# Kernel tuning notes

Hardware: AMD Instinct MI355X
Metric: run time of the kernel (lower is better)

Reference implementation:

```python
import jax, jax.numpy as jnp
import numpy as np

N = 100000      # nodes
E = 1600000     # edges
F_IN = 512      # num_feat
HID = 128       # hidden dim (hardcoded in GNN)
ENC = 64        # encoder_dim
NCLS = 10       # num_classes
DOM = 40        # domain head hidden (hardcoded)


def setup_inputs() -> dict:
    key = jax.random.key(0)
    ks = jax.random.split(key, 16)
    def lin(k, fi, fo):
        kw, kb = jax.random.split(k)
        s = 1.0 / np.sqrt(fi)
        return (jax.random.uniform(kw, (fi, fo), jnp.float32, -s, s),
                jax.random.uniform(kb, (fo,), jnp.float32, -s, s))
    W1, b1 = lin(ks[0], F_IN, HID)
    W2, b2 = lin(ks[1], HID, ENC)
    att_w, att_b = lin(ks[2], ENC, 1)
    cls_w, cls_b = lin(ks[3], ENC, NCLS)
    dw1, db1 = lin(ks[4], ENC, DOM)
    dw2, db2 = lin(ks[5], DOM, 2)
    return {
        "x": jax.random.normal(ks[6], (N, F_IN), jnp.float32),
        "edge_index": jax.random.randint(ks[7], (2, E), 0, N, jnp.int64),
        "ppmi_edge_weight": jax.random.uniform(ks[8], (E,), jnp.float32, 0.01, 1.0),
        "rate": 1,
        "W1": W1, "b1": b1, "W2": W2, "b2": b2,
        "att_w": att_w, "att_b": att_b,
        "cls_w": cls_w, "cls_b": cls_b,
        "dw1": dw1, "db1": db1, "dw2": dw2, "db2": db2,
    }


def _edge_norm(src, dst, w):
    # symmetric normalization d^-1/2 * w * d^-1/2 (self-loops already included)
    deg = jax.ops.segment_sum(w, dst, num_segments=N)
    dinv = jnp.where(deg > 0, jax.lax.rsqrt(deg), 0.0)
    return dinv[src] * w * dinv[dst]


def _conv(h, W, b, src, dst, enorm):
    h = h @ W                                   # [N, out]
    msg = h[src] * enorm[:, None]               # [E+N, out] gather
    return jax.ops.segment_sum(msg, dst, num_segments=N) + b


def _encode(x, src, dst, enorm, W1, b1, W2, b2):
    h = jax.nn.relu(_conv(x, W1, b1, src, dst, enorm))  # dropout = identity (eval)
    return _conv(h, W2, b2, src, dst, enorm)


def reference(x, edge_index, ppmi_edge_weight, rate,
              W1, b1, W2, b2, att_w, att_b,
              cls_w, cls_b, dw1, db1, dw2, db2):
    loop = jnp.arange(N, dtype=edge_index.dtype)
    src = jnp.concatenate([edge_index[0], loop])
    dst = jnp.concatenate([edge_index[1], loop])
    ones_w = jnp.ones(src.shape[0], jnp.float32)
    ppmi_w = jnp.concatenate([ppmi_edge_weight, jnp.ones(N, jnp.float32)])

    gcn_norm = _edge_norm(src, dst, ones_w)
    ppmi_norm = _edge_norm(src, dst, ppmi_w)

    # both encoders share weights (base_model=self.encoder)
    g = _encode(x, src, dst, gcn_norm, W1, b1, W2, b2)    # [N, ENC]
    p = _encode(x, src, dst, ppmi_norm, W1, b1, W2, b2)   # [N, ENC]

    stacked = jnp.stack([g, p], axis=1)                   # [N, 2, ENC]
    logits = stacked @ att_w + att_b                      # [N, 2, 1]
    wts = jax.nn.softmax(logits, axis=1)
    emb = jnp.sum(stacked * wts, axis=1)                  # [N, ENC]

    class_predict = emb @ cls_w + cls_b
    r = jnp.float32(rate)
    # gradient reversal: identity fwd, -rate * grad bwd
    rev = jax.lax.stop_gradient((1.0 + r) * emb) - r * emb
    h = jax.nn.relu(rev @ dw1 + db1)                      # dropout = identity (eval)
    domain_predict = h @ dw2 + db2
    return emb, class_predict, domain_predict
```

## Files before the change

### kernel.cpp

```cpp
#include <hip/hip_runtime.h>
#include <math.h>
#include <stdint.h>

#define NND  100000
#define NED  1600000
#define FIN  512
#define HID  128
#define ENC  64
#define NCLS 10
#define DOM  40

#define SCAN_BS 256
#define NBS ((NND + SCAN_BS - 1) / SCAN_BS)

#define NGEMM 1563
#define NDEG  521
#define NPH1  (NGEMM + NDEG)

typedef __attribute__((ext_vector_type(8))) short short8v;
typedef __attribute__((ext_vector_type(8))) unsigned short ushort8v;
typedef __attribute__((ext_vector_type(4))) float f32x4;
typedef __attribute__((ext_vector_type(4))) unsigned int uint4v;


__device__ inline void split8(const float4 a, const float4 b,
                              short8v& hi, short8v& lo) {
  float f[8] = {a.x, a.y, a.z, a.w, b.x, b.y, b.z, b.w};
  uint4v H, L;
#pragma unroll
  for (int i = 0; i < 4; ++i) {
    unsigned int u0 = __float_as_uint(f[2 * i]);
    unsigned int u1 = __float_as_uint(f[2 * i + 1]);
    H[i] = (u0 >> 16) | (u1 & 0xffff0000u);
    float l0 = f[2 * i]     - __uint_as_float(u0 & 0xffff0000u);
    float l1 = f[2 * i + 1] - __uint_as_float(u1 & 0xffff0000u);
    L[i] = (__float_as_uint(l0) >> 16) | (__float_as_uint(l1) & 0xffff0000u);
  }
  hi = __builtin_bit_cast(short8v, H);
  lo = __builtin_bit_cast(short8v, L);
}

__device__ inline ushort f2bf_rne(float x) {
  unsigned int u = __float_as_uint(x);
  unsigned int r = u + 0x7fffu + ((u >> 16) & 1u);
  return (ushort)(r >> 16);
}

__device__ inline float bf2f(unsigned short v) {
  return __uint_as_float((unsigned int)v << 16);
}

__device__ inline void gload_lds16(const float* gp, float* lp) {
  __builtin_amdgcn_global_load_lds(
      (const __attribute__((address_space(1))) void*)gp,
      (__attribute__((address_space(3))) void*)lp, 16, 0, 0);
}


__global__ void k_prep(const float* __restrict__ W1, ushort* __restrict__ b1hi,
                       const float* __restrict__ W2,
                       ushort* __restrict__ b2hi, ushort* __restrict__ b2lo,
                       unsigned int* __restrict__ packed, int* __restrict__ cursor) {
  int id = blockIdx.x * 256 + threadIdx.x;
  if (id == 0) *cursor = 0;
  if (id < NND) packed[id] = 0u;
  if (id < FIN * HID) {
    int k = id / HID, c = id % HID;
    size_t o = ((size_t)(k >> 3) * HID + c) * 8 + (k & 7);
    b1hi[o] = f2bf_rne(W1[id]);
  } else {
    int id2 = id - FIN * HID;
    if (id2 >= HID * ENC) return;
    int k = id2 / ENC, c = id2 % ENC;
    float x = W2[id2];
    unsigned int u = __float_as_uint(x);
    ushort h = (ushort)(u >> 16);
    float lo = x - __uint_as_float(u & 0xffff0000u);
    ushort l = (ushort)(__float_as_uint(lo) >> 16);
    size_t o = ((size_t)(k >> 3) * ENC + c) * 8 + (k & 7);
    b2hi[o] = h;
    b2lo[o] = l;
  }
}


__global__ __launch_bounds__(256, 4) void k_phase1(
    const float* __restrict__ A, const ushort* __restrict__ Bhi,
    ushort* __restrict__ C,
    const int* __restrict__ dst, const float* __restrict__ ppmi,
    unsigned int* __restrict__ packed, ushort* __restrict__ rank) {
  __shared__ float At[2][64 * 32];
  const int bi = blockIdx.x;
  const int tid = threadIdx.x;

  if ((bi & 3) == 0) {
    for (int e = (bi >> 2) * 256 + tid; e < NED; e += NDEG * 256) {
      int d = dst[e];
      unsigned int fx = (unsigned int)(ppmi[e] * 262144.0f + 0.5f);
      unsigned int v = (1u << 25) | fx;
      unsigned int old = atomicAdd(&packed[d], v);
      rank[e] = (ushort)(old >> 25);
    }
    return;
  }

  const int gb = bi - (bi >> 2) - 1;
  const int lane = tid & 63;
  const int w = tid >> 6;
  const int wr = w >> 1, wc = w & 1;
  const int g = lane >> 4;
  const int l16 = lane & 15;
  const int row_base = gb * 64;

  size_t srow[2]; int scol[2];
#pragma unroll
  for (int i = 0; i < 2; ++i) {
    int ee = i * 1024 + tid * 4;
    int r = ee >> 5;
    int chunk_lds = (ee >> 2) & 7;
    int chunk_g = chunk_lds ^ (r & 7);
    int rr = row_base + r; if (rr >= NND) rr = NND - 1;
    srow[i] = (size_t)rr * FIN;
    scol[i] = chunk_g * 4;
  }

  int coln[4];
#pragma unroll
  for (int n = 0; n < 4; ++n) coln[n] = wc * 64 + n * 16 + l16;
  int arow_l[2];
#pragma unroll
  for (int m = 0; m < 2; ++m) arow_l[m] = wr * 32 + m * 16 + l16;

  f32x4 acc[2][4] = {};

#pragma unroll
  for (int i = 0; i < 2; ++i)
    gload_lds16(A + srow[i] + 0 + scol[i], &At[0][i * 1024 + tid * 4]);
  __syncthreads();

  for (int t = 0; t < FIN / 32; ++t) {
    const int cur = t & 1;
    if (t + 1 < FIN / 32) {
      const int k0n = (t + 1) * 32;
#pragma unroll
      for (int i = 0; i < 2; ++i)
        gload_lds16(A + srow[i] + k0n + scol[i], &At[cur ^ 1][i * 1024 + tid * 4]);
    }

    short8v ah[2], al[2];
#pragma unroll
    for (int m = 0; m < 2; ++m) {
      int r = arow_l[m];
      int c0 = (((g * 2)     ^ (r & 7)) << 2);
      int c1 = (((g * 2 + 1) ^ (r & 7)) << 2);
      float4 a0 = *(const float4*)&At[cur][r * 32 + c0];
      float4 a1 = *(const float4*)&At[cur][r * 32 + c1];
      split8(a0, a1, ah[m], al[m]);
    }

    short8v bh[4];
    const int kc = t * 4 + g;
#pragma unroll
    for (int n = 0; n < 4; ++n)
      bh[n] = *(const short8v*)(Bhi + ((size_t)kc * HID + coln[n]) * 8);

#pragma unroll
    for (int m = 0; m < 2; ++m)
#pragma unroll
      for (int n = 0; n < 4; ++n) {
        acc[m][n] = __builtin_amdgcn_mfma_f32_16x16x32_bf16(ah[m], bh[n], acc[m][n], 0, 0, 0);
        acc[m][n] = __builtin_amdgcn_mfma_f32_16x16x32_bf16(al[m], bh[n], acc[m][n], 0, 0, 0);
      }

    __syncthreads();
  }

#pragma unroll
  for (int m = 0; m < 2; ++m)
#pragma unroll
    for (int i = 0; i < 4; ++i) {
      int r = row_base + wr * 32 + m * 16 + g * 4 + i;
      if (r < NND) {
#pragma unroll
        for (int n = 0; n < 4; ++n)
          C[(size_t)r * HID + coln[n]] = f2bf_rne(acc[m][n][i]);
      }
    }
}


__global__ void k_dinv_alloc(const unsigned int* __restrict__ packed,
                             float* __restrict__ dinv_g, float* __restrict__ dinv_p,
                             int* __restrict__ row_ptr, int* __restrict__ cursor) {
  __shared__ int s[SCAN_BS];
  __shared__ int base;
  int t = threadIdx.x, i = blockIdx.x * SCAN_BS + t;
  int cnt = 0;
  if (i < NND) {
    unsigned int pk = packed[i];
    cnt = (int)(pk >> 25);
    float dp = (float)(pk & 0x1FFFFFFu) * (1.0f / 262144.0f);
    dinv_g[i] = 1.0f / sqrtf((float)cnt + 1.0f);
    dinv_p[i] = 1.0f / sqrtf(dp + 1.0f);
  }
  s[t] = cnt;
  __syncthreads();
  for (int o = 1; o < SCAN_BS; o <<= 1) {
    int add = (t >= o) ? s[t - o] : 0;
    __syncthreads();
    s[t] += add;
    __syncthreads();
  }
  if (t == SCAN_BS - 1) base = atomicAdd(cursor, s[t]);
  __syncthreads();
  if (i < NND) row_ptr[i] = base + s[t] - cnt;
}


__global__ void k_scatter(const int* __restrict__ src, const int* __restrict__ dst,
                          const float* __restrict__ ppmi,
                          const int* __restrict__ row_ptr, const ushort* __restrict__ rank,
                          const float* __restrict__ dinv_g, const float* __restrict__ dinv_p,
                          int2* __restrict__ csr) {
  int e = blockIdx.x * blockDim.x + threadIdx.x;
  if (e >= NED) return;
  int s = src[e], d = dst[e];
  int pos = row_ptr[d] + (int)rank[e];
  ushort gn = f2bf_rne(dinv_g[s] * dinv_g[d]);
  ushort pn = f2bf_rne(dinv_p[s] * ppmi[e] * dinv_p[d]);
  int2 rec;
  rec.x = s;
  rec.y = (int)gn | ((int)pn << 16);
  csr[pos] = rec;
}


__global__ __launch_bounds__(256, 4) void gemm2_split(
    const ushort* __restrict__ As, const ushort* __restrict__ Bhi,
    const ushort* __restrict__ Blo, ushort* __restrict__ C,
    int M, int K, int Nc) {
  const int lane = threadIdx.x & 63;
  const int w = threadIdx.x >> 6;
  const int g = lane >> 4;
  const int l16 = lane & 15;
  const int row_base = blockIdx.x * 128 + w * 32;

  size_t arow[2];
#pragma unroll
  for (int m = 0; m < 2; ++m) {
    int r = row_base + m * 16 + l16;
    if (r >= M) r = M - 1;
    arow[m] = (size_t)r * K;
  }
  int coln[4];
#pragma unroll
  for (int n = 0; n < 4; ++n) coln[n] = n * 16 + l16;

  f32x4 acc[2][4] = {};

  for (int k0 = 0; k0 < K; k0 += 32) {
    short8v ah[2];
#pragma unroll
    for (int m = 0; m < 2; ++m)
      ah[m] = *(const short8v*)(As + arow[m] + k0 + g * 8);
    short8v bh[4], bl[4];
    const int kc = (k0 >> 3) + g;
#pragma unroll
    for (int n = 0; n < 4; ++n) {
      size_t off = ((size_t)kc * Nc + coln[n]) * 8;
      bh[n] = *(const short8v*)(Bhi + off);
      bl[n] = *(const short8v*)(Blo + off);
    }
#pragma unroll
    for (int m = 0; m < 2; ++m)
#pragma unroll
      for (int n = 0; n < 4; ++n) {
        acc[m][n] = __builtin_amdgcn_mfma_f32_16x16x32_bf16(ah[m], bh[n], acc[m][n], 0, 0, 0);
        acc[m][n] = __builtin_amdgcn_mfma_f32_16x16x32_bf16(ah[m], bl[n], acc[m][n], 0, 0, 0);
      }
  }

#pragma unroll
  for (int m = 0; m < 2; ++m)
#pragma unroll
    for (int i = 0; i < 4; ++i) {
      int r = row_base + m * 16 + g * 4 + i;
      if (r < M) {
#pragma unroll
        for (int n = 0; n < 4; ++n) {
          int c = coln[n];
          size_t o = (r < NND) ? ((size_t)r * 128 + c)
                               : ((size_t)(r - NND) * 128 + 64 + c);
          C[o] = f2bf_rne(acc[m][n][i]);
        }
      }
    }
}


__global__ __launch_bounds__(256) void k_agg1(
    const ushort* __restrict__ hlinb, const int* __restrict__ row_ptr,
    const unsigned int* __restrict__ packed, const int2* __restrict__ csr,
    const float* __restrict__ dinv_g, const float* __restrict__ dinv_p,
    const float* __restrict__ b1, ushort* __restrict__ hhs) {
  int wid = (blockIdx.x * blockDim.x + threadIdx.x) >> 6;
  int lane = threadIdx.x & 63;
  if (wid >= NND) return;
  const int gp = lane >> 4;
  const int t  = lane & 15;
  float sg = dinv_g[wid]; sg *= sg;
  float sp = dinv_p[wid]; sp *= sp;

  float ag[8] = {}, ap[8] = {};
  if (gp == 0) {
    ushort8v v = *(const ushort8v*)(hlinb + (size_t)wid * HID + 8 * t);
#pragma unroll
    for (int i = 0; i < 8; ++i) {
      float f = bf2f(v[i]);
      ag[i] = f * sg; ap[i] = f * sp;
    }
  }
  int e0 = row_ptr[wid];
  int e1 = e0 + (int)(packed[wid] >> 25);
  int k = e0 + gp;
  if (k < e1) {
    int2 rec = csr[k];
    while (true) {
      int kn = k + 4;
      int2 nrec = csr[kn < e1 ? kn : k];
      float wg = bf2f((ushort)(rec.y & 0xffff));
      float wp = bf2f((ushort)((unsigned)rec.y >> 16));
      ushort8v u = *(const ushort8v*)(hlinb + (size_t)rec.x * HID + 8 * t);
#pragma unroll
      for (int i = 0; i < 8; ++i) {
        float f = bf2f(u[i]);
        ag[i] = fmaf(f, wg, ag[i]);
        ap[i] = fmaf(f, wp, ap[i]);
      }
      if (kn >= e1) break;
      k = kn; rec = nrec;
    }
  }
#pragma unroll
  for (int i = 0; i < 8; ++i) {
    ag[i] += __shfl_xor(ag[i], 32); ap[i] += __shfl_xor(ap[i], 32);
    ag[i] += __shfl_xor(ag[i], 16); ap[i] += __shfl_xor(ap[i], 16);
  }

  float bb[8];
  *(float4*)&bb[0] = *(const float4*)(b1 + 8 * t);
  *(float4*)&bb[4] = *(const float4*)(b1 + 8 * t + 4);
  if (gp == 0 || gp == 2) {
    ushort8v outv;
#pragma unroll
    for (int i = 0; i < 8; ++i) {
      float v = (gp == 0) ? fmaxf(ag[i] + bb[i], 0.f) : fmaxf(ap[i] + bb[i], 0.f);
      outv[i] = f2bf_rne(v);
    }
    size_t row = (gp == 0) ? (size_t)wid : (size_t)(NND + wid);
    *(ushort8v*)(hhs + row * HID + 8 * t) = outv;
  }
}


__global__ __launch_bounds__(256) void k_agg2(
    const ushort* __restrict__ h2b, const int* __restrict__ row_ptr,
    const unsigned int* __restrict__ packed, const int2* __restrict__ csr,
    const float* __restrict__ dinv_g, const float* __restrict__ dinv_p,
    const float* __restrict__ b2, const float* __restrict__ att_w,
    const float* __restrict__ att_b, float* __restrict__ out_emb) {
  int wid = (blockIdx.x * blockDim.x + threadIdx.x) >> 6;
  int lane = threadIdx.x & 63;
  if (wid >= NND) return;
  const int gp = lane >> 4;
  const int t  = lane & 15;
  const int br = t >> 3;
  const int f0 = (t & 7) * 8;
  float sg = dinv_g[wid]; sg *= sg;
  float sp = dinv_p[wid]; sp *= sp;
  const float sw = br ? sp : sg;

  float acc[8] = {};
  if (gp == 0) {
    ushort8v v = *(const ushort8v*)(h2b + (size_t)wid * 128 + 8 * t);
#pragma unroll
    for (int i = 0; i < 8; ++i) acc[i] = bf2f(v[i]) * sw;
  }
  int e0 = row_ptr[wid];
  int e1 = e0 + (int)(packed[wid] >> 25);
  int k = e0 + gp;
  if (k < e1) {
    int2 rec = csr[k];
    while (true) {
      int kn = k + 4;
      int2 nrec = csr[kn < e1 ? kn : k];
      float w = br ? bf2f((ushort)((unsigned)rec.y >> 16))
                   : bf2f((ushort)(rec.y & 0xffff));
      ushort8v u = *(const ushort8v*)(h2b + (size_t)rec.x * 128 + 8 * t);
#pragma unroll
      for (int i = 0; i < 8; ++i) acc[i] = fmaf(bf2f(u[i]), w, acc[i]);
      if (kn >= e1) break;
      k = kn; rec = nrec;
    }
  }
#pragma unroll
  for (int i = 0; i < 8; ++i) {
    acc[i] += __shfl_xor(acc[i], 32);
    acc[i] += __shfl_xor(acc[i], 16);
  }

  float bb[8];
  *(float4*)&bb[0] = *(const float4*)(b2 + f0);
  *(float4*)&bb[4] = *(const float4*)(b2 + f0 + 4);
  float v[8];
#pragma unroll
  for (int i = 0; i < 8; ++i) v[i] = acc[i] + bb[i];

  float aw[8];
  *(float4*)&aw[0] = *(const float4*)(att_w + f0);
  *(float4*)&aw[4] = *(const float4*)(att_w + f0 + 4);
  float part = 0.f;
#pragma unroll
  for (int i = 0; i < 8; ++i) part = fmaf(v[i], aw[i], part);
  part += __shfl_xor(part, 4);
  part += __shfl_xor(part, 2);
  part += __shfl_xor(part, 1);
  float other = __shfl_xor(part, 8);
  float ab = att_b[0];
  float lg = (br ? other : part) + ab;
  float lp = (br ? part : other) + ab;
  float mx = fmaxf(lg, lp);
  float eg = expf(lg - mx), ep2 = expf(lp - mx);
  float wsm = eg / (eg + ep2);

  float ov[8];
#pragma unroll
  for (int i = 0; i < 8; ++i) ov[i] = __shfl_xor(v[i], 8);
  if (gp == 0 && br == 0) {
    float4* dst = (float4*)(out_emb + (size_t)wid * 64 + f0);
    float4 o0, o1;
    o0.x = wsm * v[0] + (1.f - wsm) * ov[0];
    o0.y = wsm * v[1] + (1.f - wsm) * ov[1];
    o0.z = wsm * v[2] + (1.f - wsm) * ov[2];
    o0.w = wsm * v[3] + (1.f - wsm) * ov[3];
    o1.x = wsm * v[4] + (1.f - wsm) * ov[4];
    o1.y = wsm * v[5] + (1.f - wsm) * ov[5];
    o1.z = wsm * v[6] + (1.f - wsm) * ov[6];
    o1.w = wsm * v[7] + (1.f - wsm) * ov[7];
    dst[0] = o0;
    dst[1] = o1;
  }
}


__global__ __launch_bounds__(128) void k_head(
    const float* __restrict__ emb,
    const float* __restrict__ cls_w, const float* __restrict__ cls_b,
    const float* __restrict__ dw1, const float* __restrict__ db1,
    const float* __restrict__ dw2, const float* __restrict__ db2,
    float* __restrict__ out_cls, float* __restrict__ out_dom) {
  __shared__ float se[128 * 65];
  const int t = threadIdx.x;
  const int base = blockIdx.x * 128;
  for (int c = 0; c < 64; ++c) {
    int idx = c * 128 + t;
    int nl = idx >> 6, k = idx & 63;
    size_t g = (size_t)base * ENC + idx;
    float v = (g < (size_t)NND * ENC) ? emb[g] : 0.f;
    se[nl * 65 + k] = v;
  }
  __syncthreads();

  int node = base + t;
  float c[NCLS], hd[DOM];
#pragma unroll
  for (int j = 0; j < NCLS; ++j) c[j] = cls_b[j];
#pragma unroll
  for (int j = 0; j < DOM; ++j) hd[j] = db1[j];

  for (int k = 0; k < ENC; ++k) {
    float ev = se[t * 65 + k];
#pragma unroll
    for (int j = 0; j < NCLS; ++j) c[j] += ev * cls_w[k * NCLS + j];
#pragma unroll
    for (int j = 0; j < DOM; ++j) hd[j] += ev * dw1[k * DOM + j];
  }
  float d0 = db2[0], d1 = db2[1];
#pragma unroll
  for (int j = 0; j < DOM; ++j) {
    float hv = fmaxf(hd[j], 0.f);
    d0 += hv * dw2[j * 2];
    d1 += hv * dw2[j * 2 + 1];
  }
  if (node < NND) {
#pragma unroll
    for (int j = 0; j < NCLS; ++j) out_cls[(size_t)node * NCLS + j] = c[j];
    out_dom[(size_t)node * 2]     = d0;
    out_dom[(size_t)node * 2 + 1] = d1;
  }
}


extern "C" void kernel_launch(void* const* d_in, const int* in_sizes, int n_in,
                              void* d_out, int out_size, void* d_ws, size_t ws_size,
                              hipStream_t stream) {
  const float* x     = (const float*)d_in[0];
  const int*   ei    = (const int*)d_in[1];
  const float* ppmi  = (const float*)d_in[2];
  const float* W1    = (const float*)d_in[4];
  const float* b1    = (const float*)d_in[5];
  const float* W2    = (const float*)d_in[6];
  const float* b2    = (const float*)d_in[7];
  const float* att_w = (const float*)d_in[8];
  const float* att_b = (const float*)d_in[9];
  const float* cls_w = (const float*)d_in[10];
  const float* cls_b = (const float*)d_in[11];
  const float* dw1   = (const float*)d_in[12];
  const float* db1   = (const float*)d_in[13];
  const float* dw2   = (const float*)d_in[14];
  const float* db2   = (const float*)d_in[15];

  const int* src = ei;
  const int* dst = ei + NED;

  uintptr_t p = (uintptr_t)d_ws;
  auto alloc = [&](size_t bytes) -> void* {
    void* r = (void*)p;
    p += (bytes + 255) & ~(size_t)255;
    return r;
  };
  unsigned int* packed = (unsigned int*)alloc((size_t)NND * 4);
  int*    cursor  = (int*)   alloc(256);
  ushort* rank    = (ushort*)alloc((size_t)NED * 2);
  int*    row_ptr = (int*)   alloc((size_t)(NND + 1) * 4);
  float*  dinv_g  = (float*) alloc((size_t)NND * 4);
  float*  dinv_p  = (float*) alloc((size_t)NND * 4);
  int2*   csr     = (int2*)  alloc((size_t)NED * 8);
  ushort* b1hi    = (ushort*)alloc((size_t)FIN * HID * 2);
  ushort* b2hi    = (ushort*)alloc((size_t)HID * ENC * 2);
  ushort* b2lo    = (ushort*)alloc((size_t)HID * ENC * 2);
  ushort* h2b     = (ushort*)alloc((size_t)NND * HID * 2);
  ushort* hhs     = (ushort*)alloc((size_t)2 * NND * HID * 2);

  float* out_emb = (float*)d_out;
  float* out_cls = (float*)d_out + (size_t)NND * ENC;
  float* out_dom = (float*)d_out + (size_t)NND * (ENC + NCLS);

  ushort* h_linb = (ushort*)d_out;

  k_prep<<<(NND + 255) / 256, 256, 0, stream>>>(W1, b1hi, W2, b2hi, b2lo,
                                                packed, cursor);

  k_phase1<<<NPH1, 256, 0, stream>>>(x, b1hi, h_linb, dst, ppmi, packed, rank);

  k_dinv_alloc<<<NBS, SCAN_BS, 0, stream>>>(packed, dinv_g, dinv_p, row_ptr, cursor);
  k_scatter<<<NED / 256, 256, 0, stream>>>(src, dst, ppmi, row_ptr, rank,
                                           dinv_g, dinv_p, csr);

  k_agg1<<<(NND * 64) / 256, 256, 0, stream>>>(h_linb, row_ptr, packed, csr,
                                               dinv_g, dinv_p, b1, hhs);
  gemm2_split<<<(2 * NND + 127) / 128, 256, 0, stream>>>(
      hhs, b2hi, b2lo, h2b, 2 * NND, HID, ENC);
  k_agg2<<<(NND * 64) / 256, 256, 0, stream>>>(h2b, row_ptr, packed, csr,
                                               dinv_g, dinv_p, b2, att_w, att_b, out_emb);

  k_head<<<(NND + 127) / 128, 128, 0, stream>>>(out_emb, cls_w, cls_b, dw1, db1,
                                                dw2, db2, out_cls, out_dom);
}
```

Baseline: 385.0 us.

## Slice hidden features into 16-column planes for cache-local layer-1 aggregation

The first GEMM now writes its bf16 output as 8 column slices of 16 features each (slice-major, node-minor). The layer-1 aggregation is reworked so each block handles one slice, with two lanes per node walking all of that node's edges serially. This keeps each gathered slice (about 3.2 MB) small enough to stay cache-resident. gemm2 is adapted to read the sliced hhs layout, and phase1's launch-bounds occupancy hint is raised from 4 to 5. In exchange, the CSR is re-read 8 times, each node's edge loop is serial with no cross-lane split (so high-degree nodes cause imbalance), and raising occupancy may cause register spills.

```diff
diff --git a/kernel.cpp b/kernel.cpp
--- a/kernel.cpp
+++ b/kernel.cpp
@@ -84,7 +84,7 @@
 }
 
 
-__global__ __launch_bounds__(256, 4) void k_phase1(
+__global__ __launch_bounds__(256, 5) void k_phase1(
     const float* __restrict__ A, const ushort* __restrict__ Bhi,
     ushort* __restrict__ C,
     const int* __restrict__ dst, const float* __restrict__ ppmi,
@@ -183,7 +183,7 @@
       if (r < NND) {
 #pragma unroll
         for (int n = 0; n < 4; ++n)
-          C[(size_t)r * HID + coln[n]] = f2bf_rne(acc[m][n][i]);
+          C[((size_t)(wc * 4 + n) * NND + r) * 16 + l16] = f2bf_rne(acc[m][n][i]);
       }
     }
 }
@@ -235,6 +235,66 @@
 }
 
 
+__global__ __launch_bounds__(256) void k_agg1(
+    const ushort* __restrict__ hs, const int* __restrict__ row_ptr,
+    const unsigned int* __restrict__ packed, const int2* __restrict__ csr,
+    const float* __restrict__ dinv_g, const float* __restrict__ dinv_p,
+    const float* __restrict__ b1, ushort* __restrict__ hhs) {
+  const int s  = blockIdx.x & 7;
+  const int nb = blockIdx.x >> 3;
+  const int lane = threadIdx.x & 63;
+  const int w = threadIdx.x >> 6;
+  const int node = nb * 128 + w * 32 + (lane >> 1);
+  const int half = lane & 1;
+  if (node >= NND) return;
+
+  const ushort* hsl = hs + (size_t)s * NND * 16;
+  float sg = dinv_g[node]; sg *= sg;
+  float sp = dinv_p[node]; sp *= sp;
+
+  float ag[8], ap[8];
+  {
+    ushort8v v = *(const ushort8v*)(hsl + (size_t)node * 16 + half * 8);
+#pragma unroll
+    for (int i = 0; i < 8; ++i) {
+      float f = bf2f(v[i]);
+      ag[i] = f * sg; ap[i] = f * sp;
+    }
+  }
+  int e0 = row_ptr[node];
+  int e1 = e0 + (int)(packed[node] >> 25);
+  if (e0 < e1) {
+    int2 rec = csr[e0];
+    for (int k = e0; k < e1; ++k) {
+      int kn = k + 1;
+      int2 nrec = csr[kn < e1 ? kn : k];
+      float wg = bf2f((ushort)(rec.y & 0xffff));
+      float wp = bf2f((ushort)((unsigned)rec.y >> 16));
+      ushort8v u = *(const ushort8v*)(hsl + (size_t)rec.x * 16 + half * 8);
+#pragma unroll
+      for (int i = 0; i < 8; ++i) {
+        float f = bf2f(u[i]);
+        ag[i] = fmaf(f, wg, ag[i]);
+        ap[i] = fmaf(f, wp, ap[i]);
+      }
+      rec = nrec;
+    }
+  }
+  float bb[8];
+  *(float4*)&bb[0] = *(const float4*)(b1 + s * 16 + half * 8);
+  *(float4*)&bb[4] = *(const float4*)(b1 + s * 16 + half * 8 + 4);
+  ushort8v og, op;
+#pragma unroll
+  for (int i = 0; i < 8; ++i) {
+    og[i] = f2bf_rne(fmaxf(ag[i] + bb[i], 0.f));
+    op[i] = f2bf_rne(fmaxf(ap[i] + bb[i], 0.f));
+  }
+  size_t o = ((size_t)s * NND + node) * 16 + half * 8;
+  *(ushort8v*)(hhs + o) = og;
+  *(ushort8v*)(hhs + (size_t)8 * NND * 16 + o) = op;
+}
+
+
 __global__ __launch_bounds__(256, 4) void gemm2_split(
     const ushort* __restrict__ As, const ushort* __restrict__ Bhi,
     const ushort* __restrict__ Blo, ushort* __restrict__ C,
@@ -245,13 +305,16 @@
   const int l16 = lane & 15;
   const int row_base = blockIdx.x * 128 + w * 32;
 
-  size_t arow[2];
+  size_t abase[2];
 #pragma unroll
   for (int m = 0; m < 2; ++m) {
     int r = row_base + m * 16 + l16;
     if (r >= M) r = M - 1;
-    arow[m] = (size_t)r * K;
-  }
+    int bsel = r >= NND;
+    int nd = r - bsel * NND;
+    abase[m] = ((size_t)bsel * 8 * NND + nd) * 16 + (g & 1) * 8;
+  }
+  const size_t sl_stride = (size_t)NND * 16;
   int coln[4];
 #pragma unroll
   for (int n = 0; n < 4; ++n) coln[n] = n * 16 + l16;
@@ -259,10 +322,11 @@
   f32x4 acc[2][4] = {};
 
   for (int k0 = 0; k0 < K; k0 += 32) {
+    const int sl = (k0 >> 4) + (g >> 1);
     short8v ah[2];
 #pragma unroll
     for (int m = 0; m < 2; ++m)
-      ah[m] = *(const short8v*)(As + arow[m] + k0 + g * 8);
+      ah[m] = *(const short8v*)(As + abase[m] + (size_t)sl * sl_stride);
     short8v bh[4], bl[4];
     const int kc = (k0 >> 3) + g;
 #pragma unroll
@@ -295,71 +359,6 @@
         }
       }
     }
-}
-
-
-__global__ __launch_bounds__(256) void k_agg1(
-    const ushort* __restrict__ hlinb, const int* __restrict__ row_ptr,
-    const unsigned int* __restrict__ packed, const int2* __restrict__ csr,
-    const float* __restrict__ dinv_g, const float* __restrict__ dinv_p,
-    const float* __restrict__ b1, ushort* __restrict__ hhs) {
-  int wid = (blockIdx.x * blockDim.x + threadIdx.x) >> 6;
-  int lane = threadIdx.x & 63;
-  if (wid >= NND) return;
-  const int gp = lane >> 4;
-  const int t  = lane & 15;
-  float sg = dinv_g[wid]; sg *= sg;
-  float sp = dinv_p[wid]; sp *= sp;
-
-  float ag[8] = {}, ap[8] = {};
-  if (gp == 0) {
-    ushort8v v = *(const ushort8v*)(hlinb + (size_t)wid * HID + 8 * t);
-#pragma unroll
-    for (int i = 0; i < 8; ++i) {
-      float f = bf2f(v[i]);
-      ag[i] = f * sg; ap[i] = f * sp;
-    }
-  }
-  int e0 = row_ptr[wid];
-  int e1 = e0 + (int)(packed[wid] >> 25);
-  int k = e0 + gp;
-  if (k < e1) {
-    int2 rec = csr[k];
-    while (true) {
-      int kn = k + 4;
-      int2 nrec = csr[kn < e1 ? kn : k];
-      float wg = bf2f((ushort)(rec.y & 0xffff));
-      float wp = bf2f((ushort)((unsigned)rec.y >> 16));
-      ushort8v u = *(const ushort8v*)(hlinb + (size_t)rec.x * HID + 8 * t);
-#pragma unroll
-      for (int i = 0; i < 8; ++i) {
-        float f = bf2f(u[i]);
-        ag[i] = fmaf(f, wg, ag[i]);
-        ap[i] = fmaf(f, wp, ap[i]);
-      }
-      if (kn >= e1) break;
-      k = kn; rec = nrec;
-    }
-  }
-#pragma unroll
-  for (int i = 0; i < 8; ++i) {
-    ag[i] += __shfl_xor(ag[i], 32); ap[i] += __shfl_xor(ap[i], 32);
-    ag[i] += __shfl_xor(ag[i], 16); ap[i] += __shfl_xor(ap[i], 16);
-  }
-
-  float bb[8];
-  *(float4*)&bb[0] = *(const float4*)(b1 + 8 * t);
-  *(float4*)&bb[4] = *(const float4*)(b1 + 8 * t + 4);
-  if (gp == 0 || gp == 2) {
-    ushort8v outv;
-#pragma unroll
-    for (int i = 0; i < 8; ++i) {
-      float v = (gp == 0) ? fmaxf(ag[i] + bb[i], 0.f) : fmaxf(ap[i] + bb[i], 0.f);
-      outv[i] = f2bf_rne(v);
-    }
-    size_t row = (gp == 0) ? (size_t)wid : (size_t)(NND + wid);
-    *(ushort8v*)(hhs + row * HID + 8 * t) = outv;
-  }
 }
 
 
@@ -557,8 +556,8 @@
   k_scatter<<<NED / 256, 256, 0, stream>>>(src, dst, ppmi, row_ptr, rank,
                                            dinv_g, dinv_p, csr);
 
-  k_agg1<<<(NND * 64) / 256, 256, 0, stream>>>(h_linb, row_ptr, packed, csr,
-                                               dinv_g, dinv_p, b1, hhs);
+  k_agg1<<<8 * ((NND + 127) / 128), 256, 0, stream>>>(
+      h_linb, row_ptr, packed, csr, dinv_g, dinv_p, b1, hhs);
   gemm2_split<<<(2 * NND + 127) / 128, 256, 0, stream>>>(
       hhs, b2hi, b2lo, h2b, 2 * NND, HID, ENC);
   k_agg2<<<(NND * 64) / 256, 256, 0, stream>>>(h2b, row_ptr, packed, csr,
```

New measurement: 548.6 us. 42.5% more time.
